# Optimization experiments

Hardware: AMD Instinct MI355X
Metric: run time of the kernel (lower is better)

Reference implementation:

```python
import jax, jax.numpy as jnp
import numpy as np

E = 1024  # hidden_size
H = 16    # num_heads
D = E // H  # head_dim = 64


def setup_inputs() -> dict:
    key = jax.random.key(0)
    ks = jax.random.split(key, 10)
    s = 1.0 / np.sqrt(E)
    inp = {
        "hidden_states": jax.random.normal(ks[0], (2, 2048, E), dtype=jnp.float32),
        "attention_mask": jnp.ones((2, 2048), dtype=jnp.float32),
        "Wq": jax.random.normal(ks[1], (E, E), dtype=jnp.float32) * s,
        "bq": jnp.zeros((E,), dtype=jnp.float32),
        "Wk": jax.random.normal(ks[2], (E, E), dtype=jnp.float32) * s,
        "bk": jnp.zeros((E,), dtype=jnp.float32),
        "Wv": jax.random.normal(ks[3], (E, E), dtype=jnp.float32) * s,
        "bv": jnp.zeros((E,), dtype=jnp.float32),
        "Wo": jax.random.normal(ks[4], (E, E), dtype=jnp.float32) * s,
        "bo": jnp.zeros((E,), dtype=jnp.float32),
    }
    return inp


def _split_heads(x):
    # [B, S, E] -> [B, H, S, D]
    b, s, _ = x.shape
    return x.reshape(b, s, H, D).transpose(0, 2, 1, 3)


def reference(hidden_states, attention_mask, Wq, bq, Wk, bk, Wv, bv, Wo, bo):
    b, s, _ = hidden_states.shape
    q = _split_heads(hidden_states @ Wq + bq)  # [B,H,S,D]
    k = _split_heads(hidden_states @ Wk + bk)
    v = _split_heads(hidden_states @ Wv + bv)
    scores = jnp.einsum('bhqd,bhkd->bhqk', q, k) / jnp.sqrt(jnp.float32(D))
    scores = scores + (1.0 - attention_mask)[:, None, None, :] * -10000.0
    probs = jax.nn.softmax(scores, axis=-1)
    ctx = jnp.einsum('bhqk,bhkd->bhqd', probs, v)  # [B,H,S,D]
    ctx = ctx.transpose(0, 2, 1, 3).reshape(b, s, E)
    return ctx @ Wo + bo
```

## Files before the change

kernel.cpp:

```cpp
#include <hip/hip_runtime.h>
#include <hip/hip_bf16.h>
#include <stdint.h>

typedef __bf16 bf16x8 __attribute__((ext_vector_type(8)));
typedef __bf16 bf16x4_t __attribute__((ext_vector_type(4)));
typedef float  f32x4  __attribute__((ext_vector_type(4)));
typedef short  short8 __attribute__((ext_vector_type(8)));
typedef short  short4v __attribute__((ext_vector_type(4)));
typedef float  float4v __attribute__((ext_vector_type(4)));

#define AS1 __attribute__((address_space(1)))
#define AS3 __attribute__((address_space(3)))

__device__ __forceinline__ void g2l16(const void* g, void* l) {
    __builtin_amdgcn_global_load_lds((const AS1 void*)g, (AS3 void*)l, 16, 0, 0);
}

__device__ __forceinline__ short f2bf(float f) {
    unsigned u = __builtin_bit_cast(unsigned, f);
    unsigned r = u + 0x7FFFu + ((u >> 16) & 1u);
    return (short)(r >> 16);
}

__device__ __forceinline__ bf16x8 ldb8(const short* p) {
    return __builtin_bit_cast(bf16x8, *(const short8*)p);
}

__device__ __forceinline__ float fast_exp2(float x) {
    return __builtin_amdgcn_exp2f(x);
}

#define LOG2E 1.44269504f
#define QSCL (0.125f * LOG2E)

__global__ __launch_bounds__(256) void prep(
    const float* __restrict__ X, short* __restrict__ Xb,
    const float* __restrict__ W0, const float* __restrict__ W1,
    const float* __restrict__ W2, const float* __restrict__ W3,
    short* __restrict__ T0, short* __restrict__ T1,
    short* __restrict__ T2, short* __restrict__ T3) {
    int gb = blockIdx.x;
    if (gb < 4096) {
        int i = (gb * 256 + threadIdx.x) * 4;
        float4v v = *(const float4v*)(X + i);
        short4v o;
        o[0] = f2bf(v[0]); o[1] = f2bf(v[1]); o[2] = f2bf(v[2]); o[3] = f2bf(v[3]);
        *(short4v*)(Xb + i) = o;
        return;
    }
    int t = gb - 4096;
    int z = t >> 10, rem = t & 1023;
    int xb = rem & 31, yb = rem >> 5;
    const float* W = z == 0 ? W0 : z == 1 ? W1 : z == 2 ? W2 : W3;
    short* T = z == 0 ? T0 : z == 1 ? T1 : z == 2 ? T2 : T3;
    __shared__ float tt[32][33];
    int n0 = xb * 32, k0 = yb * 32;
    int tx = threadIdx.x & 31, ty = threadIdx.x >> 5;
#pragma unroll
    for (int i = 0; i < 4; i++)
        tt[ty + i * 8][tx] = W[(size_t)(k0 + ty + i * 8) * 1024 + n0 + tx];
    __syncthreads();
#pragma unroll
    for (int i = 0; i < 4; i++)
        T[(size_t)(n0 + ty + i * 8) * 1024 + k0 + tx] = f2bf(tt[tx][ty + i * 8]);
}

#define VROW 136
__global__ __launch_bounds__(256) void gemm_qkv(
    const short* __restrict__ Xb,
    const short* __restrict__ WqT, const short* __restrict__ WkT, const short* __restrict__ WvT,
    const float* __restrict__ bq, const float* __restrict__ bk, const float* __restrict__ bv,
    short* __restrict__ Qb, short* __restrict__ Kb, short* __restrict__ VT) {
    const int K = 1024, N = 1024;
    int mt = blockIdx.x;
    int yy = blockIdx.y;
    int mat = yy >> 3, nt = yy & 7;
    const short* Bt = mat == 0 ? WqT : mat == 1 ? WkT : WvT;
    const float* bias = mat == 0 ? bq : mat == 1 ? bk : bv;

    int tid = threadIdx.x;
    int w = tid >> 6, lane = tid & 63;
    int quad = lane >> 4, l16 = lane & 15;
    int wy = w >> 1, wx = w & 1;

    __shared__ __align__(16) short smem[128 * VROW];
    short* A_lds = smem;
    short* B_lds = smem + 4096;

    f32x4 acc[4][4];
#pragma unroll
    for (int mi = 0; mi < 4; mi++)
#pragma unroll
        for (int ni = 0; ni < 4; ni++) acc[mi][ni] = (f32x4){0.f, 0.f, 0.f, 0.f};

    int m0 = mt * 128, n0 = nt * 128;
    for (int kt = 0; kt < 32; kt++) {
        __syncthreads();
#pragma unroll
        for (int c = 0; c < 2; c++) {
            int row = w * 32 + c * 16 + (lane >> 2);
            g2l16(Xb + (size_t)(m0 + row) * K + kt * 32 + (lane & 3) * 8,
                  &A_lds[(w * 32 + c * 16) * 32]);
            g2l16(Bt + (size_t)(n0 + row) * K + kt * 32 + (lane & 3) * 8,
                  &B_lds[(w * 32 + c * 16) * 32]);
        }
        __syncthreads();
        bf16x8 af[4], bfr[4];
#pragma unroll
        for (int i = 0; i < 4; i++) {
            af[i]  = ldb8(&A_lds[(wy * 64 + i * 16 + l16) * 32 + quad * 8]);
            bfr[i] = ldb8(&B_lds[(wx * 64 + i * 16 + l16) * 32 + quad * 8]);
        }
#pragma unroll
        for (int mi = 0; mi < 4; mi++)
#pragma unroll
            for (int ni = 0; ni < 4; ni++)
                acc[mi][ni] = __builtin_amdgcn_mfma_f32_16x16x32_bf16(af[mi], bfr[ni], acc[mi][ni], 0, 0, 0);
    }

    if (mat < 2) {
        short* Cout = mat == 0 ? Qb : Kb;
        float s = mat == 0 ? QSCL : 1.0f;
#pragma unroll
        for (int ni = 0; ni < 4; ni++) {
            int col = n0 + wx * 64 + ni * 16 + l16;
            float bv_ = bias[col];
#pragma unroll
            for (int mi = 0; mi < 4; mi++)
#pragma unroll
                for (int r = 0; r < 4; r++) {
                    int row = m0 + wy * 64 + mi * 16 + quad * 4 + r;
                    Cout[(size_t)row * N + col] = f2bf((acc[mi][ni][r] + bv_) * s);
                }
        }
    } else {
        __syncthreads();
#pragma unroll
        for (int ni = 0; ni < 4; ni++) {
            int cl = wx * 64 + ni * 16 + l16;
            float bv_ = bias[n0 + cl];
#pragma unroll
            for (int mi = 0; mi < 4; mi++) {
                int ml = wy * 64 + mi * 16 + quad * 4;
                f32x4 a = acc[mi][ni];
                f32x4 av = {a[0] + bv_, a[1] + bv_, a[2] + bv_, a[3] + bv_};
                bf16x4_t ob = __builtin_convertvector(av, bf16x4_t);
                *(short4v*)&smem[cl * VROW + ml] = __builtin_bit_cast(short4v, ob);
            }
        }
        __syncthreads();
        int bb = m0 >> 11, ss0 = m0 & 2047;
        int t16 = tid & 15, cw = tid >> 4;
#pragma unroll
        for (int p = 0; p < 8; p++) {
            int cl = p * 16 + cw;
            int col = n0 + cl;
            *(short8*)&VT[(((size_t)(bb * 16)) << 17) + (size_t)col * 2048 + ss0 + t16 * 8] =
                *(const short8*)&smem[cl * VROW + t16 * 8];
        }
    }
}

__global__ __launch_bounds__(256) void gemm_out(
    const short* __restrict__ Ab, const short* __restrict__ Bt,
    const float* __restrict__ bias, float* __restrict__ C) {
    const int K = 1024, N = 1024;
    int mt = blockIdx.x, nt = blockIdx.y;
    int tid = threadIdx.x;
    int w = tid >> 6, lane = tid & 63;
    int quad = lane >> 4, l16 = lane & 15;

    __shared__ __align__(16) short A_lds[64 * 32];
    __shared__ __align__(16) short B_lds[128 * 32];

    f32x4 acc[4][2];
#pragma unroll
    for (int mi = 0; mi < 4; mi++)
#pragma unroll
        for (int ni = 0; ni < 2; ni++) acc[mi][ni] = (f32x4){0.f, 0.f, 0.f, 0.f};

    int m0 = mt * 64, n0 = nt * 128;
    for (int kt = 0; kt < 32; kt++) {
        __syncthreads();
        {
            int row = w * 16 + (lane >> 2);
            g2l16(Ab + (size_t)(m0 + row) * K + kt * 32 + (lane & 3) * 8,
                  &A_lds[(w * 16) * 32]);
        }
#pragma unroll
        for (int c = 0; c < 2; c++) {
            int row = w * 32 + c * 16 + (lane >> 2);
            g2l16(Bt + (size_t)(n0 + row) * K + kt * 32 + (lane & 3) * 8,
                  &B_lds[(w * 32 + c * 16) * 32]);
        }
        __syncthreads();
        bf16x8 af[4], bfr[2];
#pragma unroll
        for (int i = 0; i < 4; i++)
            af[i] = ldb8(&A_lds[(i * 16 + l16) * 32 + quad * 8]);
#pragma unroll
        for (int i = 0; i < 2; i++)
            bfr[i] = ldb8(&B_lds[(w * 32 + i * 16 + l16) * 32 + quad * 8]);
#pragma unroll
        for (int mi = 0; mi < 4; mi++)
#pragma unroll
            for (int ni = 0; ni < 2; ni++)
                acc[mi][ni] = __builtin_amdgcn_mfma_f32_16x16x32_bf16(af[mi], bfr[ni], acc[mi][ni], 0, 0, 0);
    }
#pragma unroll
    for (int ni = 0; ni < 2; ni++) {
        int col = n0 + w * 32 + ni * 16 + l16;
        float bv_ = bias[col];
#pragma unroll
        for (int mi = 0; mi < 4; mi++)
#pragma unroll
            for (int r = 0; r < 4; r++) {
                int row = m0 + mi * 16 + quad * 4 + r;
                C[(size_t)row * N + col] = acc[mi][ni][r] + bv_;
            }
    }
}

#define PROW 144
__global__ __launch_bounds__(512) void attn_kernel(
    const short* __restrict__ Qb, const short* __restrict__ Kb,
    const short* __restrict__ VT, const float* __restrict__ mask,
    short* __restrict__ ctx) {
    const int S = 2048, E = 1024, HH = 16;
    int g = blockIdx.x;
    int p = (g & 7) + 8 * (g >> 7);
    int qb = (g >> 3) & 15;
    int b = p >> 4, h = p & 15;

    int tid = threadIdx.x;
    int w = tid >> 6, lane = tid & 63;
    int quad = lane >> 4, l16 = lane & 15;

    __shared__ __align__(16) short K_lds[128 * 64];
    __shared__ __align__(16) short VT_lds[64 * 128];
    __shared__ __align__(16) short P_lds[8][16 * PROW];
    __shared__ int maskflag;

    if (tid == 0) maskflag = 1;
    __syncthreads();
    {
        float4v m = *(const float4v*)(mask + b * S + tid * 4);
        if (!(m[0] == 1.f && m[1] == 1.f && m[2] == 1.f && m[3] == 1.f))
            maskflag = 0;
    }
    __syncthreads();
    const bool nomask = (maskflag != 0);

    int q0 = qb * 128;

    bf16x8 qf[2];
#pragma unroll
    for (int kc = 0; kc < 2; kc++)
        qf[kc] = ldb8(Qb + (size_t)(b * S + q0 + w * 16 + l16) * E + h * 64 + kc * 32 + quad * 8);

    f32x4 O_t[4];
    float lsum = 0.f;
#pragma unroll
    for (int nd = 0; nd < 4; nd++) O_t[nd] = (f32x4){0.f, 0.f, 0.f, 0.f};

    const short* Kbase = Kb + (size_t)b * S * E + h * 64;
    const short* Vbase = VT + (size_t)(b * HH + h) * 64 * S;
    short* Pw = &P_lds[w][0];
    int rsw = l16 & 7;

    for (int kt = 0; kt < 16; kt++) {
        int k0 = kt * 128;
        __syncthreads();
#pragma unroll
        for (int c = 0; c < 2; c++) {
            int row = w * 16 + c * 8 + (lane >> 3);
            int srcb = (lane & 7) ^ (row & 7);
            g2l16(Kbase + (size_t)(k0 + row) * E + srcb * 8, &K_lds[(w * 16 + c * 8) * 64]);
        }
#pragma unroll
        for (int c = 0; c < 2; c++) {
            int rowd = w * 8 + c * 4 + (lane >> 4);
            int srcb = (lane & 15) ^ (rowd & 7);
            g2l16(Vbase + (size_t)rowd * S + k0 + srcb * 8, &VT_lds[(w * 8 + c * 4) * 128]);
        }
        __syncthreads();

        f32x4 sc[8];
#pragma unroll
        for (int ni = 0; ni < 8; ni++) sc[ni] = (f32x4){0.f, 0.f, 0.f, 0.f};
#pragma unroll
        for (int ni = 0; ni < 8; ni++) {
#pragma unroll
            for (int kc = 0; kc < 2; kc++) {
                int blk = (kc * 4 + quad) ^ rsw;
                bf16x8 kf = ldb8(&K_lds[(ni * 16 + l16) * 64 + blk * 8]);
                sc[ni] = __builtin_amdgcn_mfma_f32_16x16x32_bf16(kf, qf[kc], sc[ni], 0, 0, 0);
            }
        }

        if (!nomask) {
#pragma unroll
            for (int ni = 0; ni < 8; ni++) {
                float4v mrow = *(const float4v*)(mask + b * S + k0 + ni * 16 + quad * 4);
#pragma unroll
                for (int r = 0; r < 4; r++)
                    sc[ni][r] += (1.0f - mrow[r]) * (-10000.0f * LOG2E);
            }
        }

#pragma unroll
        for (int ni = 0; ni < 8; ni++)
#pragma unroll
            for (int r = 0; r < 4; r++) {
                float pp = fast_exp2(sc[ni][r]);
                sc[ni][r] = pp;
                lsum += pp;
            }

#pragma unroll
        for (int ni = 0; ni < 8; ni++) {
            bf16x4_t pb = __builtin_convertvector(sc[ni], bf16x4_t);
            *(short4v*)&Pw[l16 * PROW + (ni >> 2) * 72 + (ni & 3) * 16 + quad * 4] =
                __builtin_bit_cast(short4v, pb);
        }

#pragma unroll
        for (int hh = 0; hh < 2; hh++) {
#pragma unroll
            for (int ks = 0; ks < 2; ks++) {
                bf16x8 pf = ldb8(&Pw[l16 * PROW + hh * 72 + ks * 32 + quad * 8]);
#pragma unroll
                for (int nd = 0; nd < 4; nd++) {
                    int blk = hh * 8 + ((ks * 4 + quad) ^ rsw);
                    bf16x8 vf = ldb8(&VT_lds[(nd * 16 + l16) * 128 + blk * 8]);
                    O_t[nd] = __builtin_amdgcn_mfma_f32_16x16x32_bf16(vf, pf, O_t[nd], 0, 0, 0);
                }
            }
        }
    }

    {
        float l = lsum;
        l += __shfl_xor(l, 16, 64);
        l += __shfl_xor(l, 32, 64);
        float inv = l > 0.f ? 1.0f / l : 0.f;
        int row = q0 + w * 16 + l16;
#pragma unroll
        for (int nd = 0; nd < 4; nd++) {
            f32x4 o = O_t[nd];
            f32x4 os = {o[0] * inv, o[1] * inv, o[2] * inv, o[3] * inv};
            bf16x4_t ob = __builtin_convertvector(os, bf16x4_t);
            *(short4v*)&ctx[(size_t)(b * S + row) * E + h * 64 + nd * 16 + quad * 4] =
                __builtin_bit_cast(short4v, ob);
        }
    }
}

extern "C" void kernel_launch(void* const* d_in, const int* in_sizes, int n_in,
                              void* d_out, int out_size, void* d_ws, size_t ws_size,
                              hipStream_t stream) {
    const float* X    = (const float*)d_in[0];
    const float* mask = (const float*)d_in[1];
    const float* Wq   = (const float*)d_in[2];
    const float* bq   = (const float*)d_in[3];
    const float* Wk   = (const float*)d_in[4];
    const float* bk   = (const float*)d_in[5];
    const float* Wv   = (const float*)d_in[6];
    const float* bv   = (const float*)d_in[7];
    const float* Wo   = (const float*)d_in[8];
    const float* bo   = (const float*)d_in[9];
    float* out = (float*)d_out;

    char* ws = (char*)d_ws;
    short* Xb  = (short*)(ws);
    short* WqT = (short*)(ws + (8u << 20));
    short* WkT = (short*)(ws + (10u << 20));
    short* WvT = (short*)(ws + (12u << 20));
    short* WoT = (short*)(ws + (14u << 20));
    short* Qb  = (short*)(ws + (16u << 20));
    short* Kb  = (short*)(ws + (24u << 20));
    short* VT  = (short*)(ws + (32u << 20));
    short* ctx = Xb;

    prep<<<8192, 256, 0, stream>>>(X, Xb, Wq, Wk, Wv, Wo, WqT, WkT, WvT, WoT);
    gemm_qkv<<<dim3(32, 24), 256, 0, stream>>>(Xb, WqT, WkT, WvT, bq, bk, bv, Qb, Kb, VT);
    attn_kernel<<<512, 512, 0, stream>>>(Qb, Kb, VT, mask, ctx);
    gemm_out<<<dim3(64, 8), 256, 0, stream>>>(ctx, WoT, bo, out);
}
```

Before: 212.7 us.

## Double-buffer attention K/V tiles and vectorize GEMM epilogue stores via swapped MFMA

The attention kernel now uses 64-key tiles with double-buffered K/V LDS so the next tile loads while the current one computes, with one barrier per iteration instead of two. The row-sum is computed by an MFMA against a ones vector, replacing scalar accumulation and cross-lane shuffles. In the QKV and output GEMMs the MFMA operands are swapped so each lane holds four contiguous columns, allowing vectorized bias loads and 4-wide stores instead of scalar strided writes. The row-sum now comes from bf16-rounded probabilities, which shifts precision slightly, and the extra MFMA adds some compute.

After: 194.0 us. 1.1x faster.

```diff
diff --git a/kernel.cpp b/kernel.cpp
--- a/kernel.cpp
+++ b/kernel.cpp
@@ -89,51 +89,76 @@
 
     f32x4 acc[4][4];
 #pragma unroll
-    for (int mi = 0; mi < 4; mi++)
-#pragma unroll
-        for (int ni = 0; ni < 4; ni++) acc[mi][ni] = (f32x4){0.f, 0.f, 0.f, 0.f};
+    for (int i = 0; i < 4; i++)
+#pragma unroll
+        for (int j = 0; j < 4; j++) acc[i][j] = (f32x4){0.f, 0.f, 0.f, 0.f};
 
     int m0 = mt * 128, n0 = nt * 128;
-    for (int kt = 0; kt < 32; kt++) {
-        __syncthreads();
-#pragma unroll
-        for (int c = 0; c < 2; c++) {
-            int row = w * 32 + c * 16 + (lane >> 2);
-            g2l16(Xb + (size_t)(m0 + row) * K + kt * 32 + (lane & 3) * 8,
-                  &A_lds[(w * 32 + c * 16) * 32]);
-            g2l16(Bt + (size_t)(n0 + row) * K + kt * 32 + (lane & 3) * 8,
-                  &B_lds[(w * 32 + c * 16) * 32]);
-        }
-        __syncthreads();
-        bf16x8 af[4], bfr[4];
-#pragma unroll
-        for (int i = 0; i < 4; i++) {
-            af[i]  = ldb8(&A_lds[(wy * 64 + i * 16 + l16) * 32 + quad * 8]);
-            bfr[i] = ldb8(&B_lds[(wx * 64 + i * 16 + l16) * 32 + quad * 8]);
-        }
-#pragma unroll
-        for (int mi = 0; mi < 4; mi++)
+
+    if (mat < 2) {
+        for (int kt = 0; kt < 32; kt++) {
+            __syncthreads();
+#pragma unroll
+            for (int c = 0; c < 2; c++) {
+                int row = w * 32 + c * 16 + (lane >> 2);
+                g2l16(Xb + (size_t)(m0 + row) * K + kt * 32 + (lane & 3) * 8,
+                      &A_lds[(w * 32 + c * 16) * 32]);
+                g2l16(Bt + (size_t)(n0 + row) * K + kt * 32 + (lane & 3) * 8,
+                      &B_lds[(w * 32 + c * 16) * 32]);
+            }
+            __syncthreads();
+            bf16x8 af[4], bfr[4];
+#pragma unroll
+            for (int i = 0; i < 4; i++) {
+                af[i]  = ldb8(&A_lds[(wy * 64 + i * 16 + l16) * 32 + quad * 8]);
+                bfr[i] = ldb8(&B_lds[(wx * 64 + i * 16 + l16) * 32 + quad * 8]);
+            }
 #pragma unroll
             for (int ni = 0; ni < 4; ni++)
-                acc[mi][ni] = __builtin_amdgcn_mfma_f32_16x16x32_bf16(af[mi], bfr[ni], acc[mi][ni], 0, 0, 0);
-    }
-
-    if (mat < 2) {
+#pragma unroll
+                for (int mi = 0; mi < 4; mi++)
+                    acc[ni][mi] = __builtin_amdgcn_mfma_f32_16x16x32_bf16(bfr[ni], af[mi], acc[ni][mi], 0, 0, 0);
+        }
         short* Cout = mat == 0 ? Qb : Kb;
         float s = mat == 0 ? QSCL : 1.0f;
 #pragma unroll
         for (int ni = 0; ni < 4; ni++) {
-            int col = n0 + wx * 64 + ni * 16 + l16;
-            float bv_ = bias[col];
+            int c0 = n0 + wx * 64 + ni * 16 + quad * 4;
+            float4v bv4 = *(const float4v*)(bias + c0);
+#pragma unroll
+            for (int mi = 0; mi < 4; mi++) {
+                int row = m0 + wy * 64 + mi * 16 + l16;
+                f32x4 a = acc[ni][mi];
+                f32x4 av = {(a[0] + bv4[0]) * s, (a[1] + bv4[1]) * s,
+                            (a[2] + bv4[2]) * s, (a[3] + bv4[3]) * s};
+                bf16x4_t ob = __builtin_convertvector(av, bf16x4_t);
+                *(short4v*)&Cout[(size_t)row * N + c0] = __builtin_bit_cast(short4v, ob);
+            }
+        }
+    } else {
+        for (int kt = 0; kt < 32; kt++) {
+            __syncthreads();
+#pragma unroll
+            for (int c = 0; c < 2; c++) {
+                int row = w * 32 + c * 16 + (lane >> 2);
+                g2l16(Xb + (size_t)(m0 + row) * K + kt * 32 + (lane & 3) * 8,
+                      &A_lds[(w * 32 + c * 16) * 32]);
+                g2l16(Bt + (size_t)(n0 + row) * K + kt * 32 + (lane & 3) * 8,
+                      &B_lds[(w * 32 + c * 16) * 32]);
+            }
+            __syncthreads();
+            bf16x8 af[4], bfr[4];
+#pragma unroll
+            for (int i = 0; i < 4; i++) {
+                af[i]  = ldb8(&A_lds[(wy * 64 + i * 16 + l16) * 32 + quad * 8]);
+                bfr[i] = ldb8(&B_lds[(wx * 64 + i * 16 + l16) * 32 + quad * 8]);
+            }
 #pragma unroll
             for (int mi = 0; mi < 4; mi++)
 #pragma unroll
-                for (int r = 0; r < 4; r++) {
-                    int row = m0 + wy * 64 + mi * 16 + quad * 4 + r;
-                    Cout[(size_t)row * N + col] = f2bf((acc[mi][ni][r] + bv_) * s);
-                }
-        }
-    } else {
+                for (int ni = 0; ni < 4; ni++)
+                    acc[mi][ni] = __builtin_amdgcn_mfma_f32_16x16x32_bf16(af[mi], bfr[ni], acc[mi][ni], 0, 0, 0);
+        }
         __syncthreads();
 #pragma unroll
         for (int ni = 0; ni < 4; ni++) {
@@ -173,11 +198,11 @@
     __shared__ __align__(16) short A_lds[64 * 32];
     __shared__ __align__(16) short B_lds[128 * 32];
 
-    f32x4 acc[4][2];
-#pragma unroll
-    for (int mi = 0; mi < 4; mi++)
-#pragma unroll
-        for (int ni = 0; ni < 2; ni++) acc[mi][ni] = (f32x4){0.f, 0.f, 0.f, 0.f};
+    f32x4 acc[2][4];
+#pragma unroll
+    for (int ni = 0; ni < 2; ni++)
+#pragma unroll
+        for (int mi = 0; mi < 4; mi++) acc[ni][mi] = (f32x4){0.f, 0.f, 0.f, 0.f};
 
     int m0 = mt * 64, n0 = nt * 128;
     for (int kt = 0; kt < 32; kt++) {
@@ -202,26 +227,26 @@
         for (int i = 0; i < 2; i++)
             bfr[i] = ldb8(&B_lds[(w * 32 + i * 16 + l16) * 32 + quad * 8]);
 #pragma unroll
-        for (int mi = 0; mi < 4; mi++)
-#pragma unroll
-            for (int ni = 0; ni < 2; ni++)
-                acc[mi][ni] = __builtin_amdgcn_mfma_f32_16x16x32_bf16(af[mi], bfr[ni], acc[mi][ni], 0, 0, 0);
+        for (int ni = 0; ni < 2; ni++)
+#pragma unroll
+            for (int mi = 0; mi < 4; mi++)
+                acc[ni][mi] = __builtin_amdgcn_mfma_f32_16x16x32_bf16(bfr[ni], af[mi], acc[ni][mi], 0, 0, 0);
     }
 #pragma unroll
     for (int ni = 0; ni < 2; ni++) {
-        int col = n0 + w * 32 + ni * 16 + l16;
-        float bv_ = bias[col];
-#pragma unroll
-        for (int mi = 0; mi < 4; mi++)
-#pragma unroll
-            for (int r = 0; r < 4; r++) {
-                int row = m0 + mi * 16 + quad * 4 + r;
-                C[(size_t)row * N + col] = acc[mi][ni][r] + bv_;
-            }
-    }
-}
-
-#define PROW 144
+        int c0 = n0 + w * 32 + ni * 16 + quad * 4;
+        float4v bv4 = *(const float4v*)(bias + c0);
+#pragma unroll
+        for (int mi = 0; mi < 4; mi++) {
+            int row = m0 + mi * 16 + l16;
+            f32x4 a = acc[ni][mi];
+            float4v av = {a[0] + bv4[0], a[1] + bv4[1], a[2] + bv4[2], a[3] + bv4[3]};
+            *(float4v*)&C[(size_t)row * N + c0] = av;
+        }
+    }
+}
+
+#define PROW 72
 __global__ __launch_bounds__(512) void attn_kernel(
     const short* __restrict__ Qb, const short* __restrict__ Kb,
     const short* __restrict__ VT, const float* __restrict__ mask,
@@ -236,8 +261,8 @@
     int w = tid >> 6, lane = tid & 63;
     int quad = lane >> 4, l16 = lane & 15;
 
-    __shared__ __align__(16) short K_lds[128 * 64];
-    __shared__ __align__(16) short VT_lds[64 * 128];
+    __shared__ __align__(16) short K_lds[2][64 * 64];
+    __shared__ __align__(16) short VT_lds[2][64 * 64];
     __shared__ __align__(16) short P_lds[8][16 * PROW];
     __shared__ int maskflag;
 
@@ -258,8 +283,11 @@
     for (int kc = 0; kc < 2; kc++)
         qf[kc] = ldb8(Qb + (size_t)(b * S + q0 + w * 16 + l16) * E + h * 64 + kc * 32 + quad * 8);
 
+    short8 ones_s = {0x3F80, 0x3F80, 0x3F80, 0x3F80, 0x3F80, 0x3F80, 0x3F80, 0x3F80};
+    bf16x8 vones = __builtin_bit_cast(bf16x8, ones_s);
+
     f32x4 O_t[4];
-    float lsum = 0.f;
+    f32x4 lacc = (f32x4){0.f, 0.f, 0.f, 0.f};
 #pragma unroll
     for (int nd = 0; nd < 4; nd++) O_t[nd] = (f32x4){0.f, 0.f, 0.f, 0.f};
 
@@ -268,39 +296,40 @@
     short* Pw = &P_lds[w][0];
     int rsw = l16 & 7;
 
-    for (int kt = 0; kt < 16; kt++) {
-        int k0 = kt * 128;
-        __syncthreads();
-#pragma unroll
-        for (int c = 0; c < 2; c++) {
-            int row = w * 16 + c * 8 + (lane >> 3);
-            int srcb = (lane & 7) ^ (row & 7);
-            g2l16(Kbase + (size_t)(k0 + row) * E + srcb * 8, &K_lds[(w * 16 + c * 8) * 64]);
-        }
-#pragma unroll
-        for (int c = 0; c < 2; c++) {
-            int rowd = w * 8 + c * 4 + (lane >> 4);
-            int srcb = (lane & 15) ^ (rowd & 7);
-            g2l16(Vbase + (size_t)rowd * S + k0 + srcb * 8, &VT_lds[(w * 8 + c * 4) * 128]);
-        }
-        __syncthreads();
-
-        f32x4 sc[8];
-#pragma unroll
-        for (int ni = 0; ni < 8; ni++) sc[ni] = (f32x4){0.f, 0.f, 0.f, 0.f};
-#pragma unroll
-        for (int ni = 0; ni < 8; ni++) {
+    int srow = w * 8 + (lane >> 3);
+    int ssrcb = (lane & 7) ^ (srow & 7);
+
+    g2l16(Kbase + (size_t)srow * E + ssrcb * 8, &K_lds[0][(w * 8) * 64]);
+    g2l16(Vbase + (size_t)srow * S + 0 + ssrcb * 8, &VT_lds[0][(w * 8) * 64]);
+    __syncthreads();
+
+    for (int kt = 0; kt < 32; kt++) {
+        int cur = kt & 1;
+        int k0 = kt * 64;
+        if (kt < 31) {
+            int k1 = k0 + 64;
+            g2l16(Kbase + (size_t)(k1 + srow) * E + ssrcb * 8, &K_lds[cur ^ 1][(w * 8) * 64]);
+            g2l16(Vbase + (size_t)srow * S + k1 + ssrcb * 8, &VT_lds[cur ^ 1][(w * 8) * 64]);
+        }
+        const short* Kl = &K_lds[cur][0];
+        const short* Vl = &VT_lds[cur][0];
+
+        f32x4 sc[4];
+#pragma unroll
+        for (int ni = 0; ni < 4; ni++) sc[ni] = (f32x4){0.f, 0.f, 0.f, 0.f};
+#pragma unroll
+        for (int ni = 0; ni < 4; ni++) {
 #pragma unroll
             for (int kc = 0; kc < 2; kc++) {
                 int blk = (kc * 4 + quad) ^ rsw;
-                bf16x8 kf = ldb8(&K_lds[(ni * 16 + l16) * 64 + blk * 8]);
+                bf16x8 kf = ldb8(&Kl[(ni * 16 + l16) * 64 + blk * 8]);
                 sc[ni] = __builtin_amdgcn_mfma_f32_16x16x32_bf16(kf, qf[kc], sc[ni], 0, 0, 0);
             }
         }
 
         if (!nomask) {
 #pragma unroll
-            for (int ni = 0; ni < 8; ni++) {
+            for (int ni = 0; ni < 4; ni++) {
                 float4v mrow = *(const float4v*)(mask + b * S + k0 + ni * 16 + quad * 4);
 #pragma unroll
                 for (int r = 0; r < 4; r++)
@@ -309,40 +338,34 @@
         }
 
 #pragma unroll
-        for (int ni = 0; ni < 8; ni++)
-#pragma unroll
-            for (int r = 0; r < 4; r++) {
-                float pp = fast_exp2(sc[ni][r]);
-                sc[ni][r] = pp;
-                lsum += pp;
-            }
-
-#pragma unroll
-        for (int ni = 0; ni < 8; ni++) {
+        for (int ni = 0; ni < 4; ni++)
+#pragma unroll
+            for (int r = 0; r < 4; r++)
+                sc[ni][r] = fast_exp2(sc[ni][r]);
+
+#pragma unroll
+        for (int ni = 0; ni < 4; ni++) {
             bf16x4_t pb = __builtin_convertvector(sc[ni], bf16x4_t);
-            *(short4v*)&Pw[l16 * PROW + (ni >> 2) * 72 + (ni & 3) * 16 + quad * 4] =
+            *(short4v*)&Pw[l16 * PROW + ni * 16 + quad * 4] =
                 __builtin_bit_cast(short4v, pb);
         }
 
 #pragma unroll
-        for (int hh = 0; hh < 2; hh++) {
-#pragma unroll
-            for (int ks = 0; ks < 2; ks++) {
-                bf16x8 pf = ldb8(&Pw[l16 * PROW + hh * 72 + ks * 32 + quad * 8]);
-#pragma unroll
-                for (int nd = 0; nd < 4; nd++) {
-                    int blk = hh * 8 + ((ks * 4 + quad) ^ rsw);
-                    bf16x8 vf = ldb8(&VT_lds[(nd * 16 + l16) * 128 + blk * 8]);
-                    O_t[nd] = __builtin_amdgcn_mfma_f32_16x16x32_bf16(vf, pf, O_t[nd], 0, 0, 0);
-                }
-            }
-        }
+        for (int ks = 0; ks < 2; ks++) {
+            bf16x8 pf = ldb8(&Pw[l16 * PROW + ks * 32 + quad * 8]);
+            lacc = __builtin_amdgcn_mfma_f32_16x16x32_bf16(vones, pf, lacc, 0, 0, 0);
+#pragma unroll
+            for (int nd = 0; nd < 4; nd++) {
+                int blk = (ks * 4 + quad) ^ rsw;
+                bf16x8 vf = ldb8(&Vl[(nd * 16 + l16) * 64 + blk * 8]);
+                O_t[nd] = __builtin_amdgcn_mfma_f32_16x16x32_bf16(vf, pf, O_t[nd], 0, 0, 0);
+            }
+        }
+        __syncthreads();
     }
 
     {
-        float l = lsum;
-        l += __shfl_xor(l, 16, 64);
-        l += __shfl_xor(l, 32, 64);
+        float l = lacc[0];
         float inv = l > 0.f ? 1.0f / l : 0.f;
         int row = q0 + w * 16 + l16;
 #pragma unroll
```
